# Kernel tuning notes

Measured on AMD Instinct MI355X. Metric: run time of the kernel, lower is better.

Reference implementation:

```python
import jax, jax.numpy as jnp
import numpy as np

EMBED_DIM = 1024
NUM_HEADS = 16
HEAD_DIM = EMBED_DIM // NUM_HEADS
B, S = 2, 2048


def setup_inputs() -> dict:
    key = jax.random.key(0)
    ks = jax.random.split(key, 10)
    inp = {
        "query": jax.random.normal(ks[0], (B, S, EMBED_DIM), dtype=jnp.float32),
        "key": jax.random.normal(ks[1], (B, S, EMBED_DIM), dtype=jnp.float32),
        "value": jax.random.normal(ks[2], (B, S, EMBED_DIM), dtype=jnp.float32),
        # 0 => masked key position (matches attn_mask == 0 in the torch code)
        "attn_mask": jax.random.randint(ks[3], (B, S), 0, 2, dtype=jnp.int32),
        "Wq": jax.random.normal(ks[4], (EMBED_DIM, EMBED_DIM), dtype=jnp.float32) * 0.02,
        "bq": jnp.zeros((EMBED_DIM,), dtype=jnp.float32),
        "Wk": jax.random.normal(ks[5], (EMBED_DIM, EMBED_DIM), dtype=jnp.float32) * 0.02,
        "bk": jnp.zeros((EMBED_DIM,), dtype=jnp.float32),
        "Wv": jax.random.normal(ks[6], (EMBED_DIM, EMBED_DIM), dtype=jnp.float32) * 0.02,
        "bv": jnp.zeros((EMBED_DIM,), dtype=jnp.float32),
    }
    return inp


def _proj_heads(x, W, b):
    # x: [B, S, E] -> [B, H, S, D]  (nn.Linear uses x @ W.T + b)
    y = x @ W.T + b
    Bx, Sx, E = y.shape
    return y.reshape(Bx, Sx, NUM_HEADS, HEAD_DIM).transpose(0, 2, 1, 3)


def reference(query, key, value, attn_mask, Wq, bq, Wk, bk, Wv, bv):
    q = _proj_heads(query, Wq, bq)   # [B,H,S,D]
    k = _proj_heads(key, Wk, bk)     # [B,H,S,D]
    v = _proj_heads(value, Wv, bv)   # [B,H,S,D]
    inv_scale = float(EMBED_DIM) ** 0.5  # NOTE: original divides by sqrt(embed_dim), not sqrt(head_dim)
    scores = jnp.einsum("bhqd,bhkd->bhqk", q, k) / inv_scale  # [B,H,S,S]
    mask = (attn_mask == 0)[:, None, None, :]  # [B,1,1,S] -> broadcast over [B,H,S,S]
    scores = jnp.where(mask, -jnp.inf, scores)
    attn = jax.nn.softmax(scores, axis=-1)
    # dropout omitted for deterministic reference (see notes)
    out = jnp.einsum("bhqk,bhkd->bhqd", attn, v)  # [B,H,S,D]
    return out
```

## Files before the change

kernel.cpp:

```cpp
#include <hip/hip_runtime.h>
#include <hip/hip_bf16.h>

constexpr int BB = 2;
constexpr int SS = 2048;
constexpr int EE = 1024;
constexpr int HH = 16;
constexpr int DD = 64;
constexpr int MM = BB * SS;
constexpr int CX = MM * EE;
constexpr int CW = EE * EE;
#define QSCALE 0.045084220027780106f

typedef __attribute__((ext_vector_type(8))) short short8;
typedef __attribute__((ext_vector_type(4))) float floatx4;

__device__ inline short bf16bits(float x) {
    __hip_bfloat16 h = __float2bfloat16(x);
    return *reinterpret_cast<short*>(&h);
}

__device__ inline unsigned pkbf(float a, float b) {
    return (unsigned)(unsigned short)bf16bits(a) |
           ((unsigned)(unsigned short)bf16bits(b) << 16);
}

__device__ inline float fast_exp2(float x) {
#if __has_builtin(__builtin_amdgcn_exp2f)
    return __builtin_amdgcn_exp2f(x);
#else
    return exp2f(x);
#endif
}

__device__ inline void gl_lds16(const __hip_bfloat16* g, const short* l) {
    __builtin_amdgcn_global_load_lds(
        (const __attribute__((address_space(1))) void*)g,
        (__attribute__((address_space(3))) void*)l, 16, 0, 0);
}

__global__ __launch_bounds__(256) void convert_kernel(
    const float* __restrict__ x0, const float* __restrict__ x1, const float* __restrict__ x2,
    const float* __restrict__ w0, const float* __restrict__ w1, const float* __restrict__ w2,
    __hip_bfloat16* __restrict__ xb, __hip_bfloat16* __restrict__ wb)
{
    const long long e = (long long)(blockIdx.x * 256 + threadIdx.x) * 8;
    const float* src;
    __hip_bfloat16* dst;
    if (e < 3LL * CX) {
        const int z = (int)(e >> 22);
        const int off = (int)(e & (CX - 1));
        src = ((z == 0) ? x0 : (z == 1) ? x1 : x2) + off;
        dst = xb + e;
    } else {
        const long long e2 = e - 3LL * CX;
        const int z = (int)(e2 >> 20);
        const int off = (int)(e2 & (CW - 1));
        src = ((z == 0) ? w0 : (z == 1) ? w1 : w2) + off;
        dst = wb + e2;
    }
    const float4 a = reinterpret_cast<const float4*>(src)[0];
    const float4 b = reinterpret_cast<const float4*>(src)[1];
    short8 r;
    r[0] = bf16bits(a.x); r[1] = bf16bits(a.y); r[2] = bf16bits(a.z); r[3] = bf16bits(a.w);
    r[4] = bf16bits(b.x); r[5] = bf16bits(b.y); r[6] = bf16bits(b.z); r[7] = bf16bits(b.w);
    *reinterpret_cast<short8*>(dst) = r;
}

__global__ __launch_bounds__(256) void proj_gemm(
    const __hip_bfloat16* __restrict__ xb,
    const __hip_bfloat16* __restrict__ wb,
    const float* __restrict__ bq, const float* __restrict__ bk, const float* __restrict__ bv,
    __hip_bfloat16* __restrict__ qws,
    __hip_bfloat16* __restrict__ kws,
    __hip_bfloat16* __restrict__ vtws)
{
    const int which = blockIdx.z;
    const __hip_bfloat16* A = xb + (size_t)which * CX;
    const __hip_bfloat16* W = wb + (size_t)which * CW;
    const float* bias = (which == 0) ? bq : (which == 1) ? bk : bv;

    const int m0   = blockIdx.x * 128;
    const int n0   = blockIdx.y * 128;
    const int tid  = threadIdx.x;
    const int wave = tid >> 6;
    const int lane = tid & 63;
    const int l15  = lane & 15;
    const int quad = lane >> 4;
    const int wr   = wave >> 1;
    const int wc   = wave & 1;

    __shared__ __align__(16) short As[128 * 32];
    __shared__ __align__(16) short Bs[128 * 32];

    const int dpos  = (lane & 7) ^ (lane >> 3);
    const int drloc = 2 * (lane >> 3) + (dpos >> 2);
    const int dgran = (dpos & 3) * 8;

    const int rbase = (l15 >> 1) * 64;
    const int rslot = (((l15 & 1) * 4 + quad) ^ (l15 >> 1)) * 8;

    floatx4 acc[4][4] = {};

    for (int k0 = 0; k0 < EE; k0 += 32) {
        __syncthreads();
        #pragma unroll
        for (int p = 0; p < 2; ++p) {
            const int rb16 = wave * 32 + p * 16;
            gl_lds16(A + (size_t)(m0 + rb16 + drloc) * EE + k0 + dgran, &As[rb16 * 32]);
            gl_lds16(W + (size_t)(n0 + rb16 + drloc) * EE + k0 + dgran, &Bs[rb16 * 32]);
        }
        __syncthreads();

        short8 af[4], bf[4];
        #pragma unroll
        for (int mt = 0; mt < 4; ++mt)
            af[mt] = *reinterpret_cast<const short8*>(
                &As[(wr * 32 + mt * 8) * 64 + rbase + rslot]);
        #pragma unroll
        for (int nt = 0; nt < 4; ++nt)
            bf[nt] = *reinterpret_cast<const short8*>(
                &Bs[(wc * 32 + nt * 8) * 64 + rbase + rslot]);

        #pragma unroll
        for (int mt = 0; mt < 4; ++mt)
            #pragma unroll
            for (int nt = 0; nt < 4; ++nt)
                acc[mt][nt] = __builtin_amdgcn_mfma_f32_16x16x32_bf16(af[mt], bf[nt], acc[mt][nt], 0, 0, 0);
    }

    #pragma unroll
    for (int nt = 0; nt < 4; ++nt) {
        const int n = n0 + wc * 64 + nt * 16 + l15;
        const float bval = bias[n];
        const int h = n >> 6, d = n & 63;
        #pragma unroll
        for (int mt = 0; mt < 4; ++mt) {
            #pragma unroll
            for (int r = 0; r < 4; ++r) {
                const int m = m0 + wr * 64 + mt * 16 + quad * 4 + r;
                const int b = m >> 11;
                const int s = m & (SS - 1);
                float val = acc[mt][nt][r] + bval;
                if (which == 0) val *= QSCALE;
                const __hip_bfloat16 hv = __float2bfloat16(val);
                if (which == 0)
                    qws[(((size_t)b * HH + h) * SS + s) * DD + d] = hv;
                else if (which == 1)
                    kws[(((size_t)b * HH + h) * SS + s) * DD + d] = hv;
                else
                    vtws[(((size_t)b * HH + h) * DD + d) * SS + s] = hv;
            }
        }
    }
}

__global__ __launch_bounds__(256) void attn_kernel(
    const __hip_bfloat16* __restrict__ qws,
    const __hip_bfloat16* __restrict__ kws,
    const __hip_bfloat16* __restrict__ vtws,
    const int* __restrict__ amask,
    float* __restrict__ out)
{
    const int flatb = blockIdx.y * gridDim.x + blockIdx.x;
    const int bh    = 4 * (flatb & 7) + ((flatb >> 3) & 3);
    const int b     = bh >> 4;
    const int q0    = (flatb >> 5) * 128;
    const int tid  = threadIdx.x;
    const int wave = tid >> 6;
    const int lane = tid & 63;
    const int l15  = lane & 15;
    const int quad = lane >> 4;

    const __hip_bfloat16* Q  = qws  + (size_t)bh * SS * DD;
    const __hip_bfloat16* K  = kws  + (size_t)bh * SS * DD;
    const __hip_bfloat16* VT = vtws + (size_t)bh * DD * SS;
    const int* msk = amask + b * SS;

    __shared__ __align__(16) short Ks[2][64 * 64];
    __shared__ __align__(16) short Vs[2][64 * 64];
    __shared__ __align__(16) short Ps[4][32 * 64];
    __shared__ __align__(16) float Ms[SS];
    short* pw0 = Ps[wave];
    short* pw1 = Ps[wave] + 16 * 64;

    #pragma unroll
    for (int i = 0; i < 2; ++i) {
        const int j = tid + i * 256;
        const int4 m4 = reinterpret_cast<const int4*>(msk)[j];
        float4 f4;
        f4.x = (float)m4.x; f4.y = (float)m4.y; f4.z = (float)m4.z; f4.w = (float)m4.w;
        reinterpret_cast<float4*>(Ms)[j] = f4;
    }

    const int qrow = q0 + wave * 32 + l15;
    const short8 qa0 = *reinterpret_cast<const short8*>(Q + (size_t)qrow * DD + quad * 8);
    const short8 qa1 = *reinterpret_cast<const short8*>(Q + (size_t)qrow * DD + 32 + quad * 8);
    const short8 qa2 = *reinterpret_cast<const short8*>(Q + (size_t)(qrow + 16) * DD + quad * 8);
    const short8 qa3 = *reinterpret_cast<const short8*>(Q + (size_t)(qrow + 16) * DD + 32 + quad * 8);

    const int swz = l15 & 7;

    const int srow = lane >> 3;
    const int sg   = ((lane & 7) ^ srow) * 8;

    float l0 = 0.f, l1 = 0.f;
    floatx4 acc0[4] = {}, acc1[4] = {};

    #pragma unroll
    for (int p = 0; p < 2; ++p) {
        const int rb = wave * 16 + p * 8;
        gl_lds16(K + (size_t)(rb + srow) * DD + sg, &Ks[0][rb * 64]);
        gl_lds16(VT + (size_t)(rb + srow) * SS + sg, &Vs[0][rb * 64]);
    }
    __asm__ volatile("s_waitcnt vmcnt(0) lgkmcnt(0)" ::: "memory");
    __builtin_amdgcn_s_barrier();

    for (int t = 0; t < SS / 64; ++t) {
        const int cur = t & 1;

        if (t + 1 < SS / 64) {
            const int kn = (t + 1) * 64;
            #pragma unroll
            for (int p = 0; p < 2; ++p) {
                const int rb = wave * 16 + p * 8;
                gl_lds16(K + (size_t)(kn + rb + srow) * DD + sg, &Ks[cur ^ 1][rb * 64]);
                gl_lds16(VT + (size_t)(rb + srow) * SS + kn + sg, &Vs[cur ^ 1][rb * 64]);
            }
        }
        const int kt = t * 64;

        floatx4 s0[4], s1[4];
        __builtin_amdgcn_s_setprio(1);
        #pragma unroll
        for (int f = 0; f < 4; ++f) {
            const int krow = (f * 16 + l15) * 64;
            const short8 ka = *reinterpret_cast<const short8*>(&Ks[cur][krow + (quad ^ swz) * 8]);
            const short8 kb = *reinterpret_cast<const short8*>(&Ks[cur][krow + ((quad + 4) ^ swz) * 8]);
            floatx4 z = {};
            z = __builtin_amdgcn_mfma_f32_16x16x32_bf16(ka, qa0, z, 0, 0, 0);
            z = __builtin_amdgcn_mfma_f32_16x16x32_bf16(kb, qa1, z, 0, 0, 0);
            s0[f] = z;
            floatx4 w = {};
            w = __builtin_amdgcn_mfma_f32_16x16x32_bf16(ka, qa2, w, 0, 0, 0);
            w = __builtin_amdgcn_mfma_f32_16x16x32_bf16(kb, qa3, w, 0, 0, 0);
            s1[f] = w;
        }
        __builtin_amdgcn_s_setprio(0);

        #pragma unroll
        for (int f = 0; f < 4; ++f) {
            const float4 mf = *reinterpret_cast<const float4*>(&Ms[kt + f * 16 + quad * 4]);
            const float e00 = fast_exp2(s0[f][0]) * mf.x;
            const float e01 = fast_exp2(s0[f][1]) * mf.y;
            const float e02 = fast_exp2(s0[f][2]) * mf.z;
            const float e03 = fast_exp2(s0[f][3]) * mf.w;
            const float e10 = fast_exp2(s1[f][0]) * mf.x;
            const float e11 = fast_exp2(s1[f][1]) * mf.y;
            const float e12 = fast_exp2(s1[f][2]) * mf.z;
            const float e13 = fast_exp2(s1[f][3]) * mf.w;
            l0 += e00 + e01 + e02 + e03;
            l1 += e10 + e11 + e12 + e13;
            const int slot = ((2 * f + (quad >> 1)) ^ swz) * 8 + (quad & 1) * 4;
            uint2 p0; p0.x = pkbf(e00, e01); p0.y = pkbf(e02, e03);
            uint2 p1; p1.x = pkbf(e10, e11); p1.y = pkbf(e12, e13);
            *reinterpret_cast<uint2*>(pw0 + l15 * 64 + slot) = p0;
            *reinterpret_cast<uint2*>(pw1 + l15 * 64 + slot) = p1;
        }
        __asm__ volatile("s_waitcnt lgkmcnt(0)" ::: "memory");

        const short8 pa0 = *reinterpret_cast<const short8*>(pw0 + l15 * 64 + (quad ^ swz) * 8);
        const short8 pa1 = *reinterpret_cast<const short8*>(pw0 + l15 * 64 + ((quad + 4) ^ swz) * 8);
        const short8 pb0 = *reinterpret_cast<const short8*>(pw1 + l15 * 64 + (quad ^ swz) * 8);
        const short8 pb1 = *reinterpret_cast<const short8*>(pw1 + l15 * 64 + ((quad + 4) ^ swz) * 8);

        __builtin_amdgcn_s_setprio(1);
        #pragma unroll
        for (int nt = 0; nt < 4; ++nt) {
            const int vrow = (nt * 16 + l15) * 64;
            const short8 vb0 = *reinterpret_cast<const short8*>(&Vs[cur][vrow + (quad ^ swz) * 8]);
            const short8 vb1 = *reinterpret_cast<const short8*>(&Vs[cur][vrow + ((quad + 4) ^ swz) * 8]);
            acc0[nt] = __builtin_amdgcn_mfma_f32_16x16x32_bf16(pa0, vb0, acc0[nt], 0, 0, 0);
            acc0[nt] = __builtin_amdgcn_mfma_f32_16x16x32_bf16(pa1, vb1, acc0[nt], 0, 0, 0);
            acc1[nt] = __builtin_amdgcn_mfma_f32_16x16x32_bf16(pb0, vb0, acc1[nt], 0, 0, 0);
            acc1[nt] = __builtin_amdgcn_mfma_f32_16x16x32_bf16(pb1, vb1, acc1[nt], 0, 0, 0);
        }
        __builtin_amdgcn_s_setprio(0);

        if (t + 1 < SS / 64) {
            __asm__ volatile("s_waitcnt vmcnt(0)" ::: "memory");
            __builtin_amdgcn_s_barrier();
        }
    }

    l0 += __shfl_xor(l0, 16, 64); l0 += __shfl_xor(l0, 32, 64);
    l1 += __shfl_xor(l1, 16, 64); l1 += __shfl_xor(l1, 32, 64);
    float i0[4], i1[4];
    #pragma unroll
    for (int r = 0; r < 4; ++r) {
        i0[r] = 1.f / __shfl(l0, quad * 4 + r, 16);
        i1[r] = 1.f / __shfl(l1, quad * 4 + r, 16);
    }

    const size_t obase = (size_t)bh * SS * DD;
    #pragma unroll
    for (int nt = 0; nt < 4; ++nt)
        #pragma unroll
        for (int r = 0; r < 4; ++r) {
            const int qq = q0 + wave * 32 + quad * 4 + r;
            const int d  = nt * 16 + l15;
            out[obase + (size_t)qq * DD + d] = acc0[nt][r] * i0[r];
            out[obase + (size_t)(qq + 16) * DD + d] = acc1[nt][r] * i1[r];
        }
}

extern "C" void kernel_launch(void* const* d_in, const int* in_sizes, int n_in,
                              void* d_out, int out_size, void* d_ws, size_t ws_size,
                              hipStream_t stream) {
    const float* q    = (const float*)d_in[0];
    const float* k    = (const float*)d_in[1];
    const float* v    = (const float*)d_in[2];
    const int*   mask = (const int*)d_in[3];
    const float* Wq   = (const float*)d_in[4];
    const float* bq   = (const float*)d_in[5];
    const float* Wk   = (const float*)d_in[6];
    const float* bk   = (const float*)d_in[7];
    const float* Wv   = (const float*)d_in[8];
    const float* bv   = (const float*)d_in[9];
    float* out = (float*)d_out;

    __hip_bfloat16* qws  = (__hip_bfloat16*)d_ws;
    __hip_bfloat16* kws  = qws + (size_t)CX;
    __hip_bfloat16* vtws = kws + (size_t)CX;
    __hip_bfloat16* xb   = vtws + (size_t)CX;
    __hip_bfloat16* wb   = xb + (size_t)3 * CX;

    const int cvt_blocks = (3 * CX + 3 * CW) / (256 * 8);
    convert_kernel<<<dim3(cvt_blocks), 256, 0, stream>>>(q, k, v, Wq, Wk, Wv, xb, wb);
    proj_gemm<<<dim3(MM / 128, EE / 128, 3), 256, 0, stream>>>(
        xb, wb, bq, bk, bv, qws, kws, vtws);
    attn_kernel<<<dim3(SS / 128, BB * HH), 256, 0, stream>>>(
        qws, kws, vtws, mask, out);
}
```

Baseline: 211.1 us.

## Permute K rows so softmax probabilities feed PV MFMA from registers

K rows are loaded into shared memory under a permutation (sigma_row) chosen so that each lane's S accumulator values line up with the A-operand layout of the PV MFMA. The probabilities are then packed directly into register fragments, which removes the per-wave P staging buffer in shared memory, its writes and reads, and the lgkmcnt wait between them. The mask indexing is remapped to match the permutation. The cost is a less regular global access pattern for K rows, and the permutation has to be exactly right or the results are wrong.

```diff
diff --git a/kernel.cpp b/kernel.cpp
--- a/kernel.cpp
+++ b/kernel.cpp
@@ -13,6 +13,9 @@
 
 typedef __attribute__((ext_vector_type(8))) short short8;
 typedef __attribute__((ext_vector_type(4))) float floatx4;
+typedef __attribute__((ext_vector_type(4))) unsigned uintx4;
+
+union fragu { uintx4 u; short8 s; };
 
 __device__ inline short bf16bits(float x) {
     __hip_bfloat16 h = __float2bfloat16(x);
@@ -36,6 +39,10 @@
     __builtin_amdgcn_global_load_lds(
         (const __attribute__((address_space(1))) void*)g,
         (__attribute__((address_space(3))) void*)l, 16, 0, 0);
+}
+
+__device__ inline int sigma_row(int p) {
+    return (p & 0x23) | ((p & 0x0C) << 1) | ((p & 0x10) >> 2);
 }
 
 __global__ __launch_bounds__(256) void convert_kernel(
@@ -178,10 +185,7 @@
 
     __shared__ __align__(16) short Ks[2][64 * 64];
     __shared__ __align__(16) short Vs[2][64 * 64];
-    __shared__ __align__(16) short Ps[4][32 * 64];
     __shared__ __align__(16) float Ms[SS];
-    short* pw0 = Ps[wave];
-    short* pw1 = Ps[wave] + 16 * 64;
 
     #pragma unroll
     for (int i = 0; i < 2; ++i) {
@@ -202,15 +206,18 @@
 
     const int srow = lane >> 3;
     const int sg   = ((lane & 7) ^ srow) * 8;
+    const int sk0  = sigma_row(wave * 16 + srow);
+    const int sk1  = sigma_row(wave * 16 + 8 + srow);
 
     float l0 = 0.f, l1 = 0.f;
     floatx4 acc0[4] = {}, acc1[4] = {};
 
-    #pragma unroll
-    for (int p = 0; p < 2; ++p) {
-        const int rb = wave * 16 + p * 8;
-        gl_lds16(K + (size_t)(rb + srow) * DD + sg, &Ks[0][rb * 64]);
-        gl_lds16(VT + (size_t)(rb + srow) * SS + sg, &Vs[0][rb * 64]);
+    {
+        const int rb0 = wave * 16, rb1 = rb0 + 8;
+        gl_lds16(K + (size_t)sk0 * DD + sg, &Ks[0][rb0 * 64]);
+        gl_lds16(VT + (size_t)(rb0 + srow) * SS + sg, &Vs[0][rb0 * 64]);
+        gl_lds16(K + (size_t)sk1 * DD + sg, &Ks[0][rb1 * 64]);
+        gl_lds16(VT + (size_t)(rb1 + srow) * SS + sg, &Vs[0][rb1 * 64]);
     }
     __asm__ volatile("s_waitcnt vmcnt(0) lgkmcnt(0)" ::: "memory");
     __builtin_amdgcn_s_barrier();
@@ -220,12 +227,11 @@
 
         if (t + 1 < SS / 64) {
             const int kn = (t + 1) * 64;
-            #pragma unroll
-            for (int p = 0; p < 2; ++p) {
-                const int rb = wave * 16 + p * 8;
-                gl_lds16(K + (size_t)(kn + rb + srow) * DD + sg, &Ks[cur ^ 1][rb * 64]);
-                gl_lds16(VT + (size_t)(rb + srow) * SS + kn + sg, &Vs[cur ^ 1][rb * 64]);
-            }
+            const int rb0 = wave * 16, rb1 = rb0 + 8;
+            gl_lds16(K + (size_t)(kn + sk0) * DD + sg, &Ks[cur ^ 1][rb0 * 64]);
+            gl_lds16(VT + (size_t)(rb0 + srow) * SS + kn + sg, &Vs[cur ^ 1][rb0 * 64]);
+            gl_lds16(K + (size_t)(kn + sk1) * DD + sg, &Ks[cur ^ 1][rb1 * 64]);
+            gl_lds16(VT + (size_t)(rb1 + srow) * SS + kn + sg, &Vs[cur ^ 1][rb1 * 64]);
         }
         const int kt = t * 64;
 
@@ -247,9 +253,11 @@
         }
         __builtin_amdgcn_s_setprio(0);
 
+        fragu fa0, fa1, fb0, fb1;
         #pragma unroll
         for (int f = 0; f < 4; ++f) {
-            const float4 mf = *reinterpret_cast<const float4*>(&Ms[kt + f * 16 + quad * 4]);
+            const float4 mf = *reinterpret_cast<const float4*>(
+                &Ms[kt + 32 * (f >> 1) + 8 * quad + 4 * (f & 1)]);
             const float e00 = fast_exp2(s0[f][0]) * mf.x;
             const float e01 = fast_exp2(s0[f][1]) * mf.y;
             const float e02 = fast_exp2(s0[f][2]) * mf.z;
@@ -260,18 +268,14 @@
             const float e13 = fast_exp2(s1[f][3]) * mf.w;
             l0 += e00 + e01 + e02 + e03;
             l1 += e10 + e11 + e12 + e13;
-            const int slot = ((2 * f + (quad >> 1)) ^ swz) * 8 + (quad & 1) * 4;
-            uint2 p0; p0.x = pkbf(e00, e01); p0.y = pkbf(e02, e03);
-            uint2 p1; p1.x = pkbf(e10, e11); p1.y = pkbf(e12, e13);
-            *reinterpret_cast<uint2*>(pw0 + l15 * 64 + slot) = p0;
-            *reinterpret_cast<uint2*>(pw1 + l15 * 64 + slot) = p1;
-        }
-        __asm__ volatile("s_waitcnt lgkmcnt(0)" ::: "memory");
-
-        const short8 pa0 = *reinterpret_cast<const short8*>(pw0 + l15 * 64 + (quad ^ swz) * 8);
-        const short8 pa1 = *reinterpret_cast<const short8*>(pw0 + l15 * 64 + ((quad + 4) ^ swz) * 8);
-        const short8 pb0 = *reinterpret_cast<const short8*>(pw1 + l15 * 64 + (quad ^ swz) * 8);
-        const short8 pb1 = *reinterpret_cast<const short8*>(pw1 + l15 * 64 + ((quad + 4) ^ swz) * 8);
+            uintx4& da = (f < 2) ? fa0.u : fa1.u;
+            uintx4& db = (f < 2) ? fb0.u : fb1.u;
+            const int i0 = (f & 1) * 2;
+            da[i0]     = pkbf(e00, e01);
+            da[i0 + 1] = pkbf(e02, e03);
+            db[i0]     = pkbf(e10, e11);
+            db[i0 + 1] = pkbf(e12, e13);
+        }
 
         __builtin_amdgcn_s_setprio(1);
         #pragma unroll
@@ -279,10 +283,10 @@
             const int vrow = (nt * 16 + l15) * 64;
             const short8 vb0 = *reinterpret_cast<const short8*>(&Vs[cur][vrow + (quad ^ swz) * 8]);
             const short8 vb1 = *reinterpret_cast<const short8*>(&Vs[cur][vrow + ((quad + 4) ^ swz) * 8]);
-            acc0[nt] = __builtin_amdgcn_mfma_f32_16x16x32_bf16(pa0, vb0, acc0[nt], 0, 0, 0);
-            acc0[nt] = __builtin_amdgcn_mfma_f32_16x16x32_bf16(pa1, vb1, acc0[nt], 0, 0, 0);
-            acc1[nt] = __builtin_amdgcn_mfma_f32_16x16x32_bf16(pb0, vb0, acc1[nt], 0, 0, 0);
-            acc1[nt] = __builtin_amdgcn_mfma_f32_16x16x32_bf16(pb1, vb1, acc1[nt], 0, 0, 0);
+            acc0[nt] = __builtin_amdgcn_mfma_f32_16x16x32_bf16(fa0.s, vb0, acc0[nt], 0, 0, 0);
+            acc0[nt] = __builtin_amdgcn_mfma_f32_16x16x32_bf16(fa1.s, vb1, acc0[nt], 0, 0, 0);
+            acc1[nt] = __builtin_amdgcn_mfma_f32_16x16x32_bf16(fb0.s, vb0, acc1[nt], 0, 0, 0);
+            acc1[nt] = __builtin_amdgcn_mfma_f32_16x16x32_bf16(fb1.s, vb1, acc1[nt], 0, 0, 0);
         }
         __builtin_amdgcn_s_setprio(0);
 
```

Result: faster. 203.1 us (-3.8%).
